# Optimization experiments

Measured on AMD Instinct MI355X. Metric: run time of the kernel, lower is better.

## Reference

```python
import jax, jax.numpy as jnp
import numpy as np

N_HEAD = 16
ROT_DIM = 64  # partial rotary dims (< head_size=128)


def _apply_rope(x, cos, sin):
    # x: [B,H,T,R]; cos/sin: [T,R/2]. LLaMA-style pairwise complex rotation.
    x1 = x[..., 0::2]
    x2 = x[..., 1::2]
    c = cos[None, None, :, :]
    s = sin[None, None, :, :]
    o1 = x1 * c - x2 * s
    o2 = x1 * s + x2 * c
    # interleave back: [..., R/2, 2] -> [..., R]
    out = jnp.stack([o1, o2], axis=-1)
    return out.reshape(x.shape)


def setup_inputs() -> dict:
    key = jax.random.key(0)
    k1, k2, k3 = jax.random.split(key, 3)
    B, T, C = 2, 2048, 2048
    D = C // N_HEAD
    x = jax.random.normal(k1, (B, T, C), dtype=jnp.float32)
    W_attn = jax.random.normal(k2, (C, 3 * C), dtype=jnp.float32) * (1.0 / np.sqrt(C))
    W_proj = jax.random.normal(k3, (C, C), dtype=jnp.float32) * (1.0 / np.sqrt(C))
    # rotary cos/sin tables over ROT_DIM dims
    half = ROT_DIM // 2
    inv_freq = 1.0 / (10000.0 ** (np.arange(0, half, dtype=np.float32) / half))
    t = np.arange(T, dtype=np.float32)
    ang = np.outer(t, inv_freq)  # [T, R/2]
    cos = jnp.asarray(np.cos(ang), dtype=jnp.float32)
    sin = jnp.asarray(np.sin(ang), dtype=jnp.float32)
    return {"x": x, "W_attn": W_attn, "W_proj": W_proj, "cos": cos, "sin": sin}


def reference(x, W_attn, W_proj, cos, sin):
    B, T, C = x.shape
    H = N_HEAD
    D = C // H
    qkv = x @ W_attn  # [B,T,3C]
    q, k, v = jnp.split(qkv, 3, axis=-1)
    # [B,T,C] -> [B,H,T,D]
    q = q.reshape(B, T, H, D).transpose(0, 2, 1, 3)
    k = k.reshape(B, T, H, D).transpose(0, 2, 1, 3)
    v = v.reshape(B, T, H, D).transpose(0, 2, 1, 3)
    # partial RoPE on first ROT_DIM dims
    q = jnp.concatenate([_apply_rope(q[..., :ROT_DIM], cos, sin), q[..., ROT_DIM:]], axis=-1)
    k = jnp.concatenate([_apply_rope(k[..., :ROT_DIM], cos, sin), k[..., ROT_DIM:]], axis=-1)
    # bidirectional SDPA, no mask
    scale = 1.0 / jnp.sqrt(jnp.asarray(D, dtype=x.dtype))
    scores = jnp.einsum("bhqd,bhkd->bhqk", q, k) * scale
    attn = jax.nn.softmax(scores, axis=-1)
    y = jnp.einsum("bhqk,bhkd->bhqd", attn, v)  # [B,H,T,D]
    y = y.transpose(0, 2, 1, 3).reshape(B, T, C)
    return y @ W_proj
```

## Files before the change

kernel.cpp:

```cpp
#include <hip/hip_runtime.h>
#include <stdint.h>

typedef unsigned short u16;
typedef __attribute__((ext_vector_type(8))) short short8;
typedef __attribute__((ext_vector_type(4))) float f32x4;

__device__ __forceinline__ float bf2f(u16 u){
  union { uint32_t i; float f; } v; v.i = ((uint32_t)u) << 16; return v.f;
}
__device__ __forceinline__ u16 f2bf(float f){
  union { float f; uint32_t i; } v; v.f = f;
  uint32_t r = v.i + 0x7FFFu + ((v.i >> 16) & 1u);
  return (u16)(r >> 16);
}

typedef __attribute__((address_space(3))) uint32_t lds_u32;
typedef const __attribute__((address_space(1))) uint32_t gl_u32;
__device__ __forceinline__ void gl_lds16(const void* g, void* lds){
  __builtin_amdgcn_global_load_lds((gl_u32*)g, (lds_u32*)lds, 16, 0, 0);
}

__global__ void cast_f32_bf16(const float* __restrict__ src, u16* __restrict__ dst){
  const int i = blockIdx.x * 256 + threadIdx.x;
  const float4 a = ((const float4*)src)[2 * i];
  const float4 b = ((const float4*)src)[2 * i + 1];
  uint4 o;
  o.x = (uint32_t)f2bf(a.x) | ((uint32_t)f2bf(a.y) << 16);
  o.y = (uint32_t)f2bf(a.z) | ((uint32_t)f2bf(a.w) << 16);
  o.z = (uint32_t)f2bf(b.x) | ((uint32_t)f2bf(b.y) << 16);
  o.w = (uint32_t)f2bf(b.z) | ((uint32_t)f2bf(b.w) << 16);
  ((uint4*)dst)[i] = o;
}

__global__ void transpose_f32_bf16(const float* __restrict__ src, u16* __restrict__ dst,
                                   int R, int C){
  __shared__ u16 tile[32][33];
  const int cb = blockIdx.x * 32, rb = blockIdx.y * 32;
  const int tx = threadIdx.x, ty = threadIdx.y;
  #pragma unroll
  for (int i = 0; i < 32; i += 8)
    tile[ty + i][tx] = f2bf(src[(size_t)(rb + ty + i) * C + cb + tx]);
  __syncthreads();
  #pragma unroll
  for (int i = 0; i < 32; i += 8)
    dst[(size_t)(cb + ty + i) * R + rb + tx] = tile[tx][ty + i];
}

__global__ void transpose_v(const u16* __restrict__ qkv, u16* __restrict__ vT){
  __shared__ u16 tile[32][33];
  const int db = blockIdx.x * 32, tb = blockIdx.y * 32, bh = blockIdx.z;
  const int b = bh >> 4, h = bh & 15;
  const int tx = threadIdx.x, ty = threadIdx.y;
  const u16* src = qkv + (size_t)(b * 2048) * 6144 + 4096 + h * 128;
  #pragma unroll
  for (int i = 0; i < 32; i += 8) tile[ty + i][tx] = src[(size_t)(tb + ty + i) * 6144 + db + tx];
  __syncthreads();
  u16* d = vT + (size_t)bh * 128 * 2048;
  #pragma unroll
  for (int i = 0; i < 32; i += 8) d[(size_t)(db + ty + i) * 2048 + tb + tx] = tile[tx][ty + i];
}

__global__ void rope_qk(const u16* __restrict__ qkv, const float* __restrict__ cosb,
                        const float* __restrict__ sinb, u16* __restrict__ qo,
                        u16* __restrict__ ko){
  const int idx = blockIdx.x * 256 + threadIdx.x;
  const int d2 = idx & 63;
  const int h  = (idx >> 6) & 15;
  const int t  = (idx >> 10) & 2047;
  const int b  = (idx >> 21) & 1;
  const int w  = idx >> 22;
  const int incol = w * 2048 + h * 128 + 2 * d2;
  const uint32_t pair = *(const uint32_t*)(qkv + (size_t)(b * 2048 + t) * 6144 + incol);
  float x1 = bf2f((u16)(pair & 0xffff));
  float x2 = bf2f((u16)(pair >> 16));
  float o1 = x1, o2 = x2;
  if (d2 < 32){
    const float c = cosb[t * 32 + d2];
    const float s = sinb[t * 32 + d2];
    o1 = x1 * c - x2 * s;
    o2 = x1 * s + x2 * c;
  }
  const uint32_t outp = (uint32_t)f2bf(o1) | ((uint32_t)f2bf(o2) << 16);
  u16* dst = w ? ko : qo;
  *(uint32_t*)(dst + ((size_t)(b * 16 + h) * 2048 + t) * 128 + 2 * d2) = outp;
}

template<bool F32OUT>
__global__ __launch_bounds__(256) void gemm_bt(const u16* __restrict__ A,
                                               const u16* __restrict__ Bt,
                                               void* __restrict__ Cv,
                                               int M, int N, int K){
  __shared__ __align__(16) u16 sA[128 * 64];
  __shared__ __align__(16) u16 sB[128 * 64];
  const int tid  = threadIdx.x;
  const int lane = tid & 63, wave = tid >> 6;
  const int quad = lane >> 4, l15 = lane & 15;
  const int wr = wave >> 1, wc = wave & 1;
  const int mb = blockIdx.y * 128, nb = blockIdx.x * 128;

  f32x4 acc[4][4];
  #pragma unroll
  for (int i = 0; i < 4; i++)
    #pragma unroll
    for (int j = 0; j < 4; j++) acc[i][j] = (f32x4)0.0f;

  for (int k0 = 0; k0 < K; k0 += 64){
    const u16* Ab = A + (size_t)mb * K + k0;
    const u16* Bb = Bt + (size_t)nb * K + k0;
    #pragma unroll
    for (int r = 0; r < 4; r++){
      const int idx = r * 256 + tid;
      const int row = idx >> 3, c = idx & 7;
      const int gc = (c ^ (row & 7)) * 8;
      gl_lds16(Ab + (size_t)row * K + gc, (char*)sA + r * 4096 + wave * 1024);
      gl_lds16(Bb + (size_t)row * K + gc, (char*)sB + r * 4096 + wave * 1024);
    }
    __syncthreads();
    #pragma unroll
    for (int ks = 0; ks < 2; ks++){
      short8 af[4], bfr[4];
      #pragma unroll
      for (int i = 0; i < 4; i++){
        const int row = wr * 64 + i * 16 + l15;
        const int ch = (ks * 4 + quad) ^ (l15 & 7);
        af[i] = *(const short8*)((const char*)sA + row * 128 + ch * 16);
      }
      #pragma unroll
      for (int j = 0; j < 4; j++){
        const int row = wc * 64 + j * 16 + l15;
        const int ch = (ks * 4 + quad) ^ (l15 & 7);
        bfr[j] = *(const short8*)((const char*)sB + row * 128 + ch * 16);
      }
      #pragma unroll
      for (int i = 0; i < 4; i++)
        #pragma unroll
        for (int j = 0; j < 4; j++)
          acc[i][j] = __builtin_amdgcn_mfma_f32_16x16x32_bf16(af[i], bfr[j], acc[i][j], 0, 0, 0);
    }
    __syncthreads();
  }
  #pragma unroll
  for (int i = 0; i < 4; i++)
    #pragma unroll
    for (int j = 0; j < 4; j++)
      #pragma unroll
      for (int r = 0; r < 4; r++){
        const int row = mb + wr * 64 + i * 16 + quad * 4 + r;
        const int col = nb + wc * 64 + j * 16 + l15;
        if (F32OUT) ((float*)Cv)[(size_t)row * N + col] = acc[i][j][r];
        else        ((u16*)Cv)[(size_t)row * N + col]   = f2bf(acc[i][j][r]);
      }
}

__global__ __launch_bounds__(256, 4) void attn(const u16* __restrict__ q,
                                               const u16* __restrict__ k,
                                               const u16* __restrict__ vT,
                                               u16* __restrict__ y){
  __shared__ __align__(16) u16 bufK[64 * 128];
  __shared__ __align__(16) u16 bufV[128 * 64];
  __shared__ __align__(16) u16 bufP[4 * 16 * 64];
  const int tid  = threadIdx.x;
  const int lane = tid & 63, wave = tid >> 6;
  const int quad = lane >> 4, l15 = lane & 15;
  const int bh = blockIdx.x & 31, qt = blockIdx.x >> 5;
  const u16* qbh = q  + (size_t)bh * 2048 * 128;
  const u16* kbh = k  + (size_t)bh * 2048 * 128;
  const u16* vbh = vT + (size_t)bh * 128 * 2048;
  const float scale2 = 0.12754100060254310f;

  #pragma unroll
  for (int rr = 0; rr < 4; rr++){
    const int idx = rr * 256 + tid;
    const int row = idx >> 4, c = idx & 15;
    gl_lds16(qbh + (size_t)(qt * 64 + row) * 128 + ((c ^ (row & 15)) * 8),
             (char*)bufK + rr * 4096 + wave * 1024);
  }
  __syncthreads();
  short8 qf[4];
  #pragma unroll
  for (int ks = 0; ks < 4; ks++){
    const int row = wave * 16 + l15;
    const int ch = (ks * 4 + quad) ^ l15;
    qf[ks] = *(const short8*)((const char*)bufK + row * 256 + ch * 16);
  }
  __syncthreads();

  #pragma unroll
  for (int rr = 0; rr < 4; rr++){
    const int idx = rr * 256 + tid;
    const int row = idx >> 4, c = idx & 15;
    gl_lds16(kbh + (size_t)row * 128 + ((c ^ (row & 15)) * 8),
             (char*)bufK + rr * 4096 + wave * 1024);
  }
  __syncthreads();
  #pragma unroll
  for (int rr = 0; rr < 4; rr++){
    const int idx = rr * 256 + tid;
    const int row = idx >> 3, c = idx & 7;
    gl_lds16(vbh + (size_t)row * 2048 + ((c ^ (row & 7)) * 8),
             (char*)bufV + rr * 4096 + wave * 1024);
  }

  f32x4 o[8];
  #pragma unroll
  for (int ds = 0; ds < 8; ds++) o[ds] = (f32x4)0.0f;
  float l_[4] = {0.0f, 0.0f, 0.0f, 0.0f};

  for (int kt = 0; kt < 32; kt++){
    f32x4 s[4];
    #pragma unroll
    for (int kv = 0; kv < 4; kv++) s[kv] = (f32x4)0.0f;
    #pragma unroll
    for (int ks = 0; ks < 4; ks++){
      short8 bfr[4];
      #pragma unroll
      for (int kv = 0; kv < 4; kv++){
        const int row = kv * 16 + l15;
        const int ch = (ks * 4 + quad) ^ l15;
        bfr[kv] = *(const short8*)((const char*)bufK + row * 256 + ch * 16);
      }
      #pragma unroll
      for (int kv = 0; kv < 4; kv++)
        s[kv] = __builtin_amdgcn_mfma_f32_16x16x32_bf16(qf[ks], bfr[kv], s[kv], 0, 0, 0);
    }

    #pragma unroll
    for (int kv = 0; kv < 4; kv++)
      #pragma unroll
      for (int r = 0; r < 4; r++){
        const float p = exp2f(s[kv][r] * scale2);
        s[kv][r] = p;
        l_[r] += p;
      }

    __syncthreads();

    if (kt < 31){
      #pragma unroll
      for (int rr = 0; rr < 4; rr++){
        const int idx = rr * 256 + tid;
        const int row = idx >> 4, c = idx & 15;
        gl_lds16(kbh + (size_t)((kt + 1) * 64 + row) * 128 + ((c ^ (row & 15)) * 8),
                 (char*)bufK + rr * 4096 + wave * 1024);
      }
    }

    #pragma unroll
    for (int kv = 0; kv < 4; kv++)
      #pragma unroll
      for (int r = 0; r < 4; r++){
        const int row = quad * 4 + r;
        const int col = kv * 16 + l15;
        bufP[wave * 1024 + row * 64 + (((col >> 3) ^ (row & 7)) * 8) + (col & 7)]
          = f2bf(s[kv][r]);
      }

    #pragma unroll
    for (int ks = 0; ks < 2; ks++){
      const short8 pa = *(const short8*)((const char*)bufP + wave * 2048 +
                                         l15 * 128 + (((ks * 4 + quad) ^ (l15 & 7)) * 16));
      short8 vb[8];
      #pragma unroll
      for (int ds = 0; ds < 8; ds++){
        const int row = ds * 16 + l15;
        const int ch = (ks * 4 + quad) ^ (row & 7);
        vb[ds] = *(const short8*)((const char*)bufV + row * 128 + ch * 16);
      }
      #pragma unroll
      for (int ds = 0; ds < 8; ds++)
        o[ds] = __builtin_amdgcn_mfma_f32_16x16x32_bf16(pa, vb[ds], o[ds], 0, 0, 0);
    }

    __syncthreads();

    if (kt < 31){
      #pragma unroll
      for (int rr = 0; rr < 4; rr++){
        const int idx = rr * 256 + tid;
        const int row = idx >> 3, c = idx & 7;
        gl_lds16(vbh + (size_t)row * 2048 + (kt + 1) * 64 + ((c ^ (row & 7)) * 8),
                 (char*)bufV + rr * 4096 + wave * 1024);
      }
    }
  }

  #pragma unroll
  for (int r = 0; r < 4; r++){
    #pragma unroll
    for (int off = 1; off < 16; off <<= 1) l_[r] += __shfl_xor(l_[r], off);
  }

  const int b = bh >> 4, h = bh & 15;
  float inv[4];
  #pragma unroll
  for (int r = 0; r < 4; r++) inv[r] = 1.0f / l_[r];
  #pragma unroll
  for (int ds = 0; ds < 8; ds++)
    #pragma unroll
    for (int r = 0; r < 4; r++){
      const int t = qt * 64 + wave * 16 + quad * 4 + r;
      const int cc = h * 128 + ds * 16 + l15;
      y[((size_t)(b * 2048 + t)) * 2048 + cc] = f2bf(o[ds][r] * inv[r]);
    }
}

extern "C" void kernel_launch(void* const* d_in, const int* in_sizes, int n_in,
                              void* d_out, int out_size, void* d_ws, size_t ws_size,
                              hipStream_t stream) {
  const float* x    = (const float*)d_in[0];
  const float* Wa   = (const float*)d_in[1];
  const float* Wp   = (const float*)d_in[2];
  const float* cosb = (const float*)d_in[3];
  const float* sinb = (const float*)d_in[4];
  float* out = (float*)d_out;
  char* ws = (char*)d_ws;

  u16* WaT = (u16*)(ws);
  u16* WpT = (u16*)(ws + 25165824);
  u16* xb  = (u16*)(ws + 33554432);
  u16* qkv = (u16*)(ws + 50331648);
  u16* qb  = (u16*)(ws + 100663296);
  u16* kb  = (u16*)(ws + 117440512);
  u16* vTb = (u16*)(ws + 134217728);
  u16* yb  = (u16*)(ws + 33554432);

  dim3 b32(32, 8, 1);
  transpose_f32_bf16<<<dim3(192, 64, 1), b32, 0, stream>>>(Wa, WaT, 2048, 6144);
  transpose_f32_bf16<<<dim3(64, 64, 1),  b32, 0, stream>>>(Wp, WpT, 2048, 2048);
  cast_f32_bf16<<<4096, 256, 0, stream>>>(x, xb);
  gemm_bt<false><<<dim3(48, 32, 1), 256, 0, stream>>>(xb, WaT, qkv, 4096, 6144, 2048);
  rope_qk<<<32768, 256, 0, stream>>>(qkv, cosb, sinb, qb, kb);
  transpose_v<<<dim3(4, 64, 32), b32, 0, stream>>>(qkv, vTb);
  attn<<<1024, 256, 0, stream>>>(qb, kb, vTb, yb);
  gemm_bt<true><<<dim3(16, 32, 1), 256, 0, stream>>>(yb, WpT, out, 4096, 2048, 2048);
}
```

Baseline: 427.2 us.

## Use 256x256-tile pipelined GEMM with swizzled LDS for QKV projection

Adds a new 512-thread GEMM kernel with 256x256 output tiles, XOR-swizzled LDS staging via global_load_lds, double-buffered async prefetch interleaved with MFMA phases, s_setprio around the math, and a block-index swizzle for L2 locality. It replaces the 128-tile GEMM for the QKV projection only. The larger tile raises arithmetic intensity and overlaps loads with compute, at the cost of more registers and LDS per block and fewer blocks (384) on the device.

Measured after the change: 443.1 us. +3.7%, slower.

```diff
diff --git a/kernel.cpp b/kernel.cpp
--- a/kernel.cpp
+++ b/kernel.cpp
@@ -152,6 +152,120 @@
       }
 }
 
+__device__ __forceinline__ void stage8k(const u16* __restrict__ g, int ldK,
+                                        char* lds, int call, int tid){
+  const int idx = call * 512 + tid;
+  const int row = idx >> 3, c = idx & 7;
+  gl_lds16(g + (size_t)row * ldK + ((c ^ (row & 7)) * 8),
+           lds + call * 8192 + (tid >> 6) * 1024);
+}
+
+template<bool F32OUT>
+__global__ __launch_bounds__(512, 2) void gemm256_bt(const u16* __restrict__ A,
+                                                     const u16* __restrict__ Bt,
+                                                     void* __restrict__ Cv,
+                                                     int M, int N, int K){
+  __shared__ __align__(16) u16 sA[2 * 256 * 64];
+  __shared__ __align__(16) u16 sB[2 * 256 * 64];
+  const int tid  = threadIdx.x;
+  const int lane = tid & 63, wave = tid >> 6;
+  const int quad = lane >> 4, l15 = lane & 15;
+  const int wm = wave >> 2, wn = wave & 3;
+
+  const int nx = gridDim.x;
+  const int nwg = nx * gridDim.y;
+  const int bid = blockIdx.y * nx + blockIdx.x;
+  const int swz = (bid & 7) * (nwg >> 3) + (bid >> 3);
+  const int mb = (swz / nx) * 256, nb = (swz % nx) * 256;
+
+  const int NT = K >> 6;
+  const u16* Ab = A  + (size_t)mb * K;
+  const u16* Bb = Bt + (size_t)nb * K;
+
+  f32x4 acc[8][4];
+  #pragma unroll
+  for (int i = 0; i < 8; i++)
+    #pragma unroll
+    for (int n = 0; n < 4; n++) acc[i][n] = (f32x4)0.0f;
+
+  #pragma unroll
+  for (int r = 0; r < 4; r++) stage8k(Ab, K, (char*)sA, r, tid);
+  #pragma unroll
+  for (int r = 0; r < 4; r++) stage8k(Bb, K, (char*)sB, r, tid);
+  #pragma unroll
+  for (int r = 0; r < 4; r++) stage8k(Bb + 64, K, (char*)sB + 32768, r, tid);
+  asm volatile("s_waitcnt vmcnt(4)" ::: "memory");
+  __builtin_amdgcn_s_barrier();
+
+  for (int s = 0; s < NT; ++s){
+    const int cur = s & 1;
+    char* sAc = (char*)sA + cur * 32768;
+    char* sBc = (char*)sB + cur * 32768;
+    char* sAn = (char*)sA + (cur ^ 1) * 32768;
+    const u16* An = Ab + (size_t)(s + 1) * 64;
+    const u16* Bn = Bb + (size_t)(s + 2) * 64;
+    const bool pfA = (s + 1 < NT), pfB = (s + 2 < NT);
+
+    short8 bq[4][2];
+    #pragma unroll
+    for (int q = 0; q < 4; q++){
+      if (q == 0){
+        #pragma unroll
+        for (int n = 0; n < 4; n++)
+          #pragma unroll
+          for (int ks = 0; ks < 2; ks++){
+            const int row = wn * 64 + n * 16 + l15;
+            bq[n][ks] = *(const short8*)(sBc + row * 128 +
+                                         (((ks * 4 + quad) ^ (l15 & 7)) * 16));
+          }
+      }
+      short8 aq[2][2];
+      #pragma unroll
+      for (int i = 0; i < 2; i++)
+        #pragma unroll
+        for (int ks = 0; ks < 2; ks++){
+          const int row = wm * 128 + (q * 2 + i) * 16 + l15;
+          aq[i][ks] = *(const short8*)(sAc + row * 128 +
+                                       (((ks * 4 + quad) ^ (l15 & 7)) * 16));
+        }
+      if (q == 0 && pfA){ stage8k(An, K, sAn, 0, tid); stage8k(An, K, sAn, 1, tid); }
+      if (q == 1 && pfA){ stage8k(An, K, sAn, 2, tid); stage8k(An, K, sAn, 3, tid); }
+      if (q == 2 && pfB){ stage8k(Bn, K, sBc, 0, tid); stage8k(Bn, K, sBc, 1, tid); }
+      if (q == 3 && pfB){ stage8k(Bn, K, sBc, 2, tid); stage8k(Bn, K, sBc, 3, tid); }
+
+      __builtin_amdgcn_s_barrier();
+      asm volatile("s_waitcnt lgkmcnt(0)" ::: "memory");
+      __builtin_amdgcn_s_setprio(1);
+      #pragma unroll
+      for (int ks = 0; ks < 2; ks++)
+        #pragma unroll
+        for (int i = 0; i < 2; i++)
+          #pragma unroll
+          for (int n = 0; n < 4; n++)
+            acc[q * 2 + i][n] = __builtin_amdgcn_mfma_f32_16x16x32_bf16(
+                aq[i][ks], bq[n][ks], acc[q * 2 + i][n], 0, 0, 0);
+      __builtin_amdgcn_s_setprio(0);
+      if (q == 3){
+        if (pfB)      asm volatile("s_waitcnt vmcnt(4)" ::: "memory");
+        else if (pfA) asm volatile("s_waitcnt vmcnt(0)" ::: "memory");
+      }
+      __builtin_amdgcn_s_barrier();
+    }
+  }
+
+  #pragma unroll
+  for (int i = 0; i < 8; i++)
+    #pragma unroll
+    for (int n = 0; n < 4; n++)
+      #pragma unroll
+      for (int r = 0; r < 4; r++){
+        const int row = mb + wm * 128 + i * 16 + quad * 4 + r;
+        const int col = nb + wn * 64 + n * 16 + l15;
+        if (F32OUT) ((float*)Cv)[(size_t)row * N + col] = acc[i][n][r];
+        else        ((u16*)Cv)[(size_t)row * N + col]   = f2bf(acc[i][n][r]);
+      }
+}
+
 __global__ __launch_bounds__(256, 4) void attn(const u16* __restrict__ q,
                                                const u16* __restrict__ k,
                                                const u16* __restrict__ vT,
@@ -328,7 +442,7 @@
   transpose_f32_bf16<<<dim3(192, 64, 1), b32, 0, stream>>>(Wa, WaT, 2048, 6144);
   transpose_f32_bf16<<<dim3(64, 64, 1),  b32, 0, stream>>>(Wp, WpT, 2048, 2048);
   cast_f32_bf16<<<4096, 256, 0, stream>>>(x, xb);
-  gemm_bt<false><<<dim3(48, 32, 1), 256, 0, stream>>>(xb, WaT, qkv, 4096, 6144, 2048);
+  gemm256_bt<false><<<dim3(24, 16, 1), 512, 0, stream>>>(xb, WaT, qkv, 4096, 6144, 2048);
   rope_qk<<<32768, 256, 0, stream>>>(qkv, cosb, sinb, qb, kb);
   transpose_v<<<dim3(4, 64, 32), b32, 0, stream>>>(qkv, vTb);
   attn<<<1024, 256, 0, stream>>>(qb, kb, vTb, yb);
```
